# Performance work log

Measured on AMD Instinct MI355X. Metric: run time of the kernel, lower is better.

Reference implementation:

```python
import jax, jax.numpy as jnp
import numpy as np

T, N, C = 4096, 16, 512


def setup_inputs() -> dict:
    key = jax.random.key(0)
    k1, k2, k3 = jax.random.split(key, 3)
    x = jax.random.normal(k1, (T, N, C), dtype=jnp.float32)
    cached_len = jax.random.randint(k2, (N,), 0, 1000, dtype=jnp.int32)
    cached_avg = jax.random.normal(k3, (N, C), dtype=jnp.float32)
    return {"x": x, "cached_len": cached_len, "cached_avg": cached_avg}


def reference(x, cached_len, cached_avg):
    # x: (T, N, C); cached_len: (N,) int; cached_avg: (N, C)
    t = x.shape[0]
    len_f = cached_len.astype(x.dtype)  # (N,)
    # running sum including cached state
    csum = jnp.cumsum(x, axis=0) + (cached_avg * len_f[:, None])[None]  # (T,N,C)
    # per-step counts: arange(1..T) + cached_len, broadcast to (T, N, 1)
    counts = jnp.arange(1, t + 1, dtype=x.dtype)[:, None] + len_f[None, :]  # (T,N)
    new_x = csum * (1.0 / counts)[:, :, None]  # (T,N,C)
    new_cached_len = cached_len + t
    new_cached_avg = new_x[-1]
    return new_x, new_cached_len, new_cached_avg
```

## Files before the change

kernel.cpp:

```cpp
#include <hip/hip_runtime.h>

constexpr int T   = 4096;
constexpr int N   = 16;
constexpr int C   = 512;
constexpr int NC  = N * C;
constexpr int NC4 = NC / 4;
constexpr int CH  = 128;
constexpr int L   = T / CH;
constexpr int TNC = T * NC;

__global__ __launch_bounds__(256) void chunk_sums(
    const float* __restrict__ x, float* __restrict__ partial)
{
    int gid  = blockIdx.x * blockDim.x + threadIdx.x;
    int ch   = gid >> 11;
    int col4 = gid & (NC4 - 1);

    const float4* xp = reinterpret_cast<const float4*>(x);
    float4 s = make_float4(0.f, 0.f, 0.f, 0.f);
    int base = ch * L * NC4 + col4;
#pragma unroll 8
    for (int i = 0; i < L; ++i) {
        float4 v = xp[base + i * NC4];
        s.x += v.x; s.y += v.y; s.z += v.z; s.w += v.w;
    }
    reinterpret_cast<float4*>(partial)[ch * NC4 + col4] = s;
}

__global__ __launch_bounds__(256) void scan_chunks(
    float* __restrict__ partial,
    const int* __restrict__ cached_len,
    float* __restrict__ out_len)
{
    int nc = blockIdx.x * blockDim.x + threadIdx.x;
    float running = 0.f;
#pragma unroll
    for (int ch0 = 0; ch0 < CH; ch0 += 16) {
        float v[16];
#pragma unroll
        for (int i = 0; i < 16; ++i) v[i] = partial[(ch0 + i) * NC + nc];
#pragma unroll
        for (int i = 0; i < 16; ++i) {
            partial[(ch0 + i) * NC + nc] = running;
            running += v[i];
        }
    }
    if (nc < N) out_len[nc] = (float)(cached_len[nc] + T);
}

__global__ __launch_bounds__(256) void finalize(
    const float* __restrict__ x,
    const float* __restrict__ partial,
    const int* __restrict__ cached_len,
    const float* __restrict__ cached_avg,
    float* __restrict__ out,
    float* __restrict__ out_avg)
{
    int gid  = blockIdx.x * blockDim.x + threadIdx.x;
    int ch   = gid >> 11;
    int col4 = gid & (NC4 - 1);
    int n    = col4 >> 7;
    float lenf = (float)cached_len[n];

    float4 b = reinterpret_cast<const float4*>(cached_avg)[col4];
    b.x *= lenf; b.y *= lenf; b.z *= lenf; b.w *= lenf;

    const float4* xp = reinterpret_cast<const float4*>(x);
    float4 s = reinterpret_cast<const float4*>(partial)[ch * NC4 + col4];
    float4* op = reinterpret_cast<float4*>(out);

    int t0 = ch * L;
    float4 o = make_float4(0.f, 0.f, 0.f, 0.f);
#pragma unroll 8
    for (int i = 0; i < L; ++i) {
        int t = t0 + i;
        float4 v = xp[t * NC4 + col4];
        s.x += v.x; s.y += v.y; s.z += v.z; s.w += v.w;
        float r = 1.0f / ((float)(t + 1) + lenf);
        o.x = (s.x + b.x) * r;
        o.y = (s.y + b.y) * r;
        o.z = (s.z + b.z) * r;
        o.w = (s.w + b.w) * r;
        op[t * NC4 + col4] = o;
    }
    if (ch == CH - 1) {
        reinterpret_cast<float4*>(out_avg)[col4] = o;
    }
}

extern "C" void kernel_launch(void* const* d_in, const int* in_sizes, int n_in,
                              void* d_out, int out_size, void* d_ws, size_t ws_size,
                              hipStream_t stream)
{
    const float* x          = (const float*)d_in[0];
    const int*   cached_len = (const int*)d_in[1];
    const float* cached_avg = (const float*)d_in[2];

    float* out     = (float*)d_out;
    float* out_len = out + TNC;
    float* out_avg = out + TNC + N;

    float* partial = (float*)d_ws;

    chunk_sums <<<CH * NC4 / 256, 256, 0, stream>>>(x, partial);
    scan_chunks<<<NC / 256,       256, 0, stream>>>(partial, cached_len, out_len);
    finalize   <<<CH * NC4 / 256, 256, 0, stream>>>(x, partial, cached_len, cached_avg,
                                                    out, out_avg);
}
```

Measured before the change: 259.9 us.

## Fuse chunk-prefix scan into finalize kernel and halve chunk count

Removes the separate scan_chunks kernel. Each finalize block now sums the partial totals of all earlier chunks itself, which saves one launch and a serial pass over the partial buffer. The chunk count drops from 128 to 64, so each chunk covers more time steps and the redundant prefix sums stay cheap. The cost is fewer and longer per-thread serial loops in both kernels, which lowers parallelism, and redundant prefix reads that grow with the chunk index.

```diff
diff --git a/kernel.cpp b/kernel.cpp
--- a/kernel.cpp
+++ b/kernel.cpp
@@ -1,15 +1,16 @@
 #include <hip/hip_runtime.h>
 
-constexpr int T   = 4096;
-constexpr int N   = 16;
-constexpr int C   = 512;
-constexpr int NC  = N * C;
-constexpr int NC4 = NC / 4;
-constexpr int CH  = 128;
-constexpr int L   = T / CH;
-constexpr int TNC = T * NC;
+constexpr int T      = 4096;
+constexpr int N      = 16;
+constexpr int C      = 512;
+constexpr int NC     = N * C;
+constexpr int NC4    = NC / 4;
+constexpr int CH     = 64;
+constexpr int L      = T / CH;
+constexpr int TNC    = T * NC;
+constexpr int STRIPS = NC4 / 256;
 
-__global__ __launch_bounds__(256) void chunk_sums(
+__global__ __launch_bounds__(256) void pool_k1_sums(
     const float* __restrict__ x, float* __restrict__ partial)
 {
     int gid  = blockIdx.x * blockDim.x + threadIdx.x;
@@ -27,46 +28,34 @@
     reinterpret_cast<float4*>(partial)[ch * NC4 + col4] = s;
 }
 
-__global__ __launch_bounds__(256) void scan_chunks(
-    float* __restrict__ partial,
-    const int* __restrict__ cached_len,
-    float* __restrict__ out_len)
-{
-    int nc = blockIdx.x * blockDim.x + threadIdx.x;
-    float running = 0.f;
-#pragma unroll
-    for (int ch0 = 0; ch0 < CH; ch0 += 16) {
-        float v[16];
-#pragma unroll
-        for (int i = 0; i < 16; ++i) v[i] = partial[(ch0 + i) * NC + nc];
-#pragma unroll
-        for (int i = 0; i < 16; ++i) {
-            partial[(ch0 + i) * NC + nc] = running;
-            running += v[i];
-        }
-    }
-    if (nc < N) out_len[nc] = (float)(cached_len[nc] + T);
-}
-
-__global__ __launch_bounds__(256) void finalize(
+__global__ __launch_bounds__(256) void pool_k2_scan(
     const float* __restrict__ x,
     const float* __restrict__ partial,
     const int* __restrict__ cached_len,
     const float* __restrict__ cached_avg,
     float* __restrict__ out,
+    float* __restrict__ out_len,
     float* __restrict__ out_avg)
 {
-    int gid  = blockIdx.x * blockDim.x + threadIdx.x;
-    int ch   = gid >> 11;
-    int col4 = gid & (NC4 - 1);
-    int n    = col4 >> 7;
+    int blk   = blockIdx.x;
+    int ch    = blk >> 3;
+    int strip = blk & (STRIPS - 1);
+    int col4  = strip * 256 + threadIdx.x;
+    int n     = col4 >> 7;
     float lenf = (float)cached_len[n];
+
+    const float4* pp = reinterpret_cast<const float4*>(partial);
+    float4 s = make_float4(0.f, 0.f, 0.f, 0.f);
+#pragma unroll 8
+    for (int j = 0; j < ch; ++j) {
+        float4 v = pp[j * NC4 + col4];
+        s.x += v.x; s.y += v.y; s.z += v.z; s.w += v.w;
+    }
 
     float4 b = reinterpret_cast<const float4*>(cached_avg)[col4];
     b.x *= lenf; b.y *= lenf; b.z *= lenf; b.w *= lenf;
 
     const float4* xp = reinterpret_cast<const float4*>(x);
-    float4 s = reinterpret_cast<const float4*>(partial)[ch * NC4 + col4];
     float4* op = reinterpret_cast<float4*>(out);
 
     int t0 = ch * L;
@@ -83,8 +72,12 @@
         o.w = (s.w + b.w) * r;
         op[t * NC4 + col4] = o;
     }
+
     if (ch == CH - 1) {
         reinterpret_cast<float4*>(out_avg)[col4] = o;
+    }
+    if (blk == 0 && threadIdx.x < N) {
+        out_len[threadIdx.x] = (float)(cached_len[threadIdx.x] + T);
     }
 }
 
@@ -102,8 +95,7 @@
 
     float* partial = (float*)d_ws;
 
-    chunk_sums <<<CH * NC4 / 256, 256, 0, stream>>>(x, partial);
-    scan_chunks<<<NC / 256,       256, 0, stream>>>(partial, cached_len, out_len);
-    finalize   <<<CH * NC4 / 256, 256, 0, stream>>>(x, partial, cached_len, cached_avg,
-                                                    out, out_avg);
+    pool_k1_sums<<<CH * NC4 / 256, 256, 0, stream>>>(x, partial);
+    pool_k2_scan<<<CH * STRIPS,    256, 0, stream>>>(x, partial, cached_len, cached_avg,
+                                                     out, out_len, out_avg);
 }
```

After: 262.5 us. Within noise of the previous version (+1.0%).
